# Performance work log

Measured on AMD Instinct MI355X. Metric: run time of the kernel, lower is better.

The kernel has to match this reference:

```python
import jax, jax.numpy as jnp
import numpy as np

ALPHA = 0.5
MOM = 0.9            # momentum m in the recurrence
ACTIVATION = "tanh"
NUM_LAYERS = 2
CACHE = 32           # GROUP size
NK = 4               # n_kernel_feats
B, N, E = 4, 4096, 128


def _act(T):
    if ACTIVATION == "leaky-relu":
        return jax.nn.leaky_relu(T)
    elif ACTIVATION == "tanh":
        return jnp.tanh(T)
    return T


def _group_indices(N, cache, stage):
    # vectorized group_pos_to_index_v2 over all (group_nr, pos_in_group)
    m = N // cache
    o = np.arange(cache)
    s = 0 if stage == 0 else (1 << (stage - 1)) % m
    g = np.arange(m)[:, None]
    block = (g + o[None, :] * s) % m
    return jnp.asarray(block * cache + o[None, :])  # [m, cache], a permutation of 0..N-1


def _ncn_layer(X, Xa, W, stage):
    B, N, E = X.shape
    ce = E // NK
    m = N // CACHE
    idx = _group_indices(N, CACHE, stage)           # [m, cache]
    Wi = W[:E].reshape(NK, ce)
    Wj = W[E:].reshape(NK, ce)
    # gather groups: [B, m, NK, cache, ce]
    xg = jnp.moveaxis(X.reshape(B, N, NK, ce)[:, idx], 3, 2)
    xag = jnp.moveaxis(Xa.reshape(B, N, NK, ce)[:, idx], 3, 2)

    def step(carry, j):
        xi, xa = carry                               # [B, m, NK, cache, ce]
        xj = jnp.take(xi, j, axis=3)                 # [B, m, NK, ce]  (row start_j)
        sim = (jnp.einsum('bgnke,ne->bgnk', xi, Wi)
               + jnp.einsum('bgne,ne->bgn', xj, Wj)[..., None])   # [B, m, NK, cache]
        T = ALPHA * xi + (1.0 - ALPHA) * sim[..., None] * xj[:, :, :, None, :]
        F = _act(T)
        ya = MOM * xa + (1.0 - MOM) * F
        yi = MOM * xi + (1.0 - MOM) * ya
        return (yi, ya), None

    (yi, ya), _ = jax.lax.scan(step, (xg, xag), jnp.arange(CACHE))

    # scatter back; idx is a permutation so .set reproduces the += into zeros
    def scatter(v):
        v = jnp.moveaxis(v, 2, 3).reshape(B, m * CACHE, E)
        return jnp.zeros((B, N, E), v.dtype).at[:, idx.reshape(-1)].set(v)

    return scatter(yi), scatter(ya)


def setup_inputs() -> dict:
    key = jax.random.key(0)
    k1, k2, k3 = jax.random.split(key, 3)
    x = jax.random.normal(k1, (B, N, E), jnp.float32)
    xa = jax.random.normal(k2, (B, N, E), jnp.float32)
    W = jax.random.normal(k3, (NUM_LAYERS, 2 * E), jnp.float32)
    return {"x": x, "xa": xa, "W": W}


def reference(x, xa, W):
    for l in range(NUM_LAYERS):
        x, xa = _ncn_layer(x, xa, W[l], l)
    return x, xa
```

## Files before the change

kernel.cpp:

```cpp
#include <hip/hip_runtime.h>


namespace {
constexpr int kB = 4;
constexpr int kN = 4096;
constexpr int kE = 128;
constexpr int kCE = 32;
constexpr int kH  = 16;
constexpr int kQ  = kH / 2;
constexpr int kCache = 32;
constexpr int kM = kN / kCache;

typedef __attribute__((ext_vector_type(2))) float f32x2;

__device__ __forceinline__ f32x2 pk_fma(f32x2 a, f32x2 b, f32x2 c) {
    return __builtin_elementwise_fma(a, b, c);
}
}

__global__ void __launch_bounds__(64) ncn_layer_kernel(
    const float* __restrict__ x_in, const float* __restrict__ xa_in,
    const float* __restrict__ Wl,
    float* __restrict__ x_out, float* __restrict__ xa_out,
    int s)
{
    const int blk = blockIdx.x;
    const int n   = blk & 3;
    const int g   = (blk >> 2) & (kM - 1);
    const int b   = blk >> 9;
    const int t   = threadIdx.x;
    const int o   = t & 31;
    const int h   = t >> 5;

    const int r = (((g + o * s) & (kM - 1)) << 5) + o;
    const size_t base = ((size_t)(b * kN + r)) * kE + n * kCE + h * kH;

    f32x2 xi[kQ], xa[kQ], wi[kQ], wj[kQ];

    {
        const float4* xi4 = reinterpret_cast<const float4*>(x_in + base);
        const float4* xa4 = reinterpret_cast<const float4*>(xa_in + base);
        const float4* wi4 = reinterpret_cast<const float4*>(Wl + n * kCE + h * kH);
        const float4* wj4 = reinterpret_cast<const float4*>(Wl + kE + n * kCE + h * kH);
#pragma unroll
        for (int q = 0; q < kQ / 2; ++q) {
            float4 v = xi4[q];
            xi[2 * q + 0] = f32x2{v.x, v.y}; xi[2 * q + 1] = f32x2{v.z, v.w};
            float4 a = xa4[q];
            xa[2 * q + 0] = f32x2{a.x, a.y}; xa[2 * q + 1] = f32x2{a.z, a.w};
            float4 u = wi4[q];
            wi[2 * q + 0] = f32x2{u.x, u.y}; wi[2 * q + 1] = f32x2{u.z, u.w};
            float4 w = wj4[q];
            wj[2 * q + 0] = f32x2{w.x, w.y}; wj[2 * q + 1] = f32x2{w.z, w.w};
        }
    }

    const int srcbase = (t & 32) * 4;
    constexpr float L1 = 1.4426950408889634f;

#pragma unroll 4
    for (int j = 0; j < kCache; ++j) {
        const int srcaddr = srcbase + j * 4;

        f32x2 xj[kQ];
#pragma unroll
        for (int q = 0; q < kQ; ++q) {
            xj[q].x = __int_as_float(
                __builtin_amdgcn_ds_bpermute(srcaddr, __float_as_int(xi[q].x)));
            xj[q].y = __int_as_float(
                __builtin_amdgcn_ds_bpermute(srcaddr, __float_as_int(xi[q].y)));
        }

        f32x2 s01 = xi[0] * wi[0];
        f32x2 s23 = xi[1] * wi[1];
#pragma unroll
        for (int q = 2; q < kQ; q += 2) {
            s01 = pk_fma(xi[q + 0], wi[q + 0], s01);
            s23 = pk_fma(xi[q + 1], wi[q + 1], s23);
        }
#pragma unroll
        for (int q = 0; q < kQ; q += 2) {
            s01 = pk_fma(xj[q + 0], wj[q + 0], s01);
            s23 = pk_fma(xj[q + 1], wj[q + 1], s23);
        }
        f32x2 sv = s01 + s23;
        float part = sv.x + sv.y;
        float sim  = part + __shfl_xor(part, 32, 64);
        const float hv = L1 * sim;
        const f32x2 hv2 = {hv, hv};
        const f32x2 l12 = {L1, L1};
        const f32x2 one = {1.0f, 1.0f};
        const f32x2 m2  = {-2.0f, -2.0f};
        const f32x2 p1  = {0.1f, 0.1f};

#pragma unroll
        for (int q = 0; q < kQ; ++q) {
            f32x2 arg = pk_fma(xj[q], hv2, xi[q] * l12);
            f32x2 t2;
            t2.x = __builtin_amdgcn_exp2f(arg.x);
            t2.y = __builtin_amdgcn_exp2f(arg.y);
            f32x2 den = t2 + one;
            f32x2 rc;
            rc.x = __builtin_amdgcn_rcpf(den.x);
            rc.y = __builtin_amdgcn_rcpf(den.y);
            f32x2 F = pk_fma(m2, rc, one);
            xa[q] = pk_fma(p1, F - xa[q], xa[q]);
            xi[q] = pk_fma(p1, xa[q] - xi[q], xi[q]);
        }
    }

    {
        float4* xo4 = reinterpret_cast<float4*>(x_out + base);
        float4* ao4 = reinterpret_cast<float4*>(xa_out + base);
#pragma unroll
        for (int q = 0; q < kQ / 2; ++q) {
            float4 v;
            v.x = xi[2 * q + 0].x; v.y = xi[2 * q + 0].y;
            v.z = xi[2 * q + 1].x; v.w = xi[2 * q + 1].y;
            xo4[q] = v;
            float4 a;
            a.x = xa[2 * q + 0].x; a.y = xa[2 * q + 0].y;
            a.z = xa[2 * q + 1].x; a.w = xa[2 * q + 1].y;
            ao4[q] = a;
        }
    }
}

extern "C" void kernel_launch(void* const* d_in, const int* in_sizes, int n_in,
                              void* d_out, int out_size, void* d_ws, size_t ws_size,
                              hipStream_t stream) {
    const float* x  = (const float*)d_in[0];
    const float* xa = (const float*)d_in[1];
    const float* W  = (const float*)d_in[2];

    float* x_out  = (float*)d_out;
    float* xa_out = x_out + (size_t)kB * kN * kE;

    const dim3 grid(kB * kM * 4);
    const dim3 block(64);

    ncn_layer_kernel<<<grid, block, 0, stream>>>(x, xa, W, x_out, xa_out, 0);
    ncn_layer_kernel<<<grid, block, 0, stream>>>(x_out, xa_out, W + 2 * kE,
                                                 x_out, xa_out, 1);
}
```

Measured before the change: 124.1 us.

## Compute xj·Wj dot via per-row partials and bpermute, fold constants into weights

Each lane now computes its own partial dot with Wj and gathers row j's value through two bpermutes, instead of doing the dot product on the permuted xj vectors. This moves the Wj reduction off the critical path that follows the xj bpermutes. The log2(e) scale is folded into the weights at load time. The momentum update is rewritten algebraically into fewer FMAs with precomputed terms. The unroll factor is raised from 4 to 8, which may increase register pressure.

```diff
diff --git a/kernel.cpp b/kernel.cpp
--- a/kernel.cpp
+++ b/kernel.cpp
@@ -35,6 +35,8 @@
     const int r = (((g + o * s) & (kM - 1)) << 5) + o;
     const size_t base = ((size_t)(b * kN + r)) * kE + n * kCE + h * kH;
 
+    constexpr float L1 = 1.4426950408889634f;
+
     f32x2 xi[kQ], xa[kQ], wi[kQ], wj[kQ];
 
     {
@@ -49,16 +51,17 @@
             float4 a = xa4[q];
             xa[2 * q + 0] = f32x2{a.x, a.y}; xa[2 * q + 1] = f32x2{a.z, a.w};
             float4 u = wi4[q];
-            wi[2 * q + 0] = f32x2{u.x, u.y}; wi[2 * q + 1] = f32x2{u.z, u.w};
+            wi[2 * q + 0] = f32x2{u.x * L1, u.y * L1};
+            wi[2 * q + 1] = f32x2{u.z * L1, u.w * L1};
             float4 w = wj4[q];
-            wj[2 * q + 0] = f32x2{w.x, w.y}; wj[2 * q + 1] = f32x2{w.z, w.w};
+            wj[2 * q + 0] = f32x2{w.x * L1, w.y * L1};
+            wj[2 * q + 1] = f32x2{w.z * L1, w.w * L1};
         }
     }
 
     const int srcbase = (t & 32) * 4;
-    constexpr float L1 = 1.4426950408889634f;
 
-#pragma unroll 4
+#pragma unroll 8
     for (int j = 0; j < kCache; ++j) {
         const int srcaddr = srcbase + j * 4;
 
@@ -71,31 +74,47 @@
                 __builtin_amdgcn_ds_bpermute(srcaddr, __float_as_int(xi[q].y)));
         }
 
-        f32x2 s01 = xi[0] * wi[0];
-        f32x2 s23 = xi[1] * wi[1];
+        f32x2 a01 = xi[0] * wi[0];
+        f32x2 a23 = xi[1] * wi[1];
+        f32x2 b01 = xi[0] * wj[0];
+        f32x2 b23 = xi[1] * wj[1];
 #pragma unroll
         for (int q = 2; q < kQ; q += 2) {
-            s01 = pk_fma(xi[q + 0], wi[q + 0], s01);
-            s23 = pk_fma(xi[q + 1], wi[q + 1], s23);
+            a01 = pk_fma(xi[q + 0], wi[q + 0], a01);
+            a23 = pk_fma(xi[q + 1], wi[q + 1], a23);
+            b01 = pk_fma(xi[q + 0], wj[q + 0], b01);
+            b23 = pk_fma(xi[q + 1], wj[q + 1], b23);
         }
+        f32x2 av = a01 + a23;
+        f32x2 bv = b01 + b23;
+        float part = av.x + av.y;
+        float pj   = bv.x + bv.y;
+
+        float di_o = __shfl_xor(part, 32, 64);
+        float dj0  = __int_as_float(
+            __builtin_amdgcn_ds_bpermute(j * 4, __float_as_int(pj)));
+        float dj1  = __int_as_float(
+            __builtin_amdgcn_ds_bpermute(128 + j * 4, __float_as_int(pj)));
+
+        f32x2 xiL[kQ], t1[kQ], u9[kQ];
+        const f32x2 l12 = {L1, L1};
+        const f32x2 c9  = {0.9f, 0.9f};
+        const f32x2 c01 = {0.1f, 0.1f};
 #pragma unroll
-        for (int q = 0; q < kQ; q += 2) {
-            s01 = pk_fma(xj[q + 0], wj[q + 0], s01);
-            s23 = pk_fma(xj[q + 1], wj[q + 1], s23);
+        for (int q = 0; q < kQ; ++q) {
+            xiL[q] = xi[q] * l12;
+            t1[q]  = pk_fma(c9, xa[q], c01);
+            u9[q]  = xi[q] * c9;
         }
-        f32x2 sv = s01 + s23;
-        float part = sv.x + sv.y;
-        float sim  = part + __shfl_xor(part, 32, 64);
-        const float hv = L1 * sim;
-        const f32x2 hv2 = {hv, hv};
-        const f32x2 l12 = {L1, L1};
+
+        const float sim = (part + di_o) + (dj0 + dj1);
+        const f32x2 sv  = {sim, sim};
         const f32x2 one = {1.0f, 1.0f};
-        const f32x2 m2  = {-2.0f, -2.0f};
-        const f32x2 p1  = {0.1f, 0.1f};
+        const f32x2 m02 = {-0.2f, -0.2f};
 
 #pragma unroll
         for (int q = 0; q < kQ; ++q) {
-            f32x2 arg = pk_fma(xj[q], hv2, xi[q] * l12);
+            f32x2 arg = pk_fma(xj[q], sv, xiL[q]);
             f32x2 t2;
             t2.x = __builtin_amdgcn_exp2f(arg.x);
             t2.y = __builtin_amdgcn_exp2f(arg.y);
@@ -103,9 +122,8 @@
             f32x2 rc;
             rc.x = __builtin_amdgcn_rcpf(den.x);
             rc.y = __builtin_amdgcn_rcpf(den.y);
-            f32x2 F = pk_fma(m2, rc, one);
-            xa[q] = pk_fma(p1, F - xa[q], xa[q]);
-            xi[q] = pk_fma(p1, xa[q] - xi[q], xi[q]);
+            xa[q] = pk_fma(m02, rc, t1[q]);
+            xi[q] = pk_fma(c01, xa[q], u9[q]);
         }
     }
 
```

Measured after the change: 121.9 us. No clear change (-1.8%).
